# Kernel optimization log

Measured on AMD Instinct MI355X. Metric: run time of the kernel, lower is better.

Reference implementation:

```python
import jax, jax.numpy as jnp
import numpy as np

B, N, C_IN, C_OUT, E_DIM = 16, 1024, 64, 64, 4


def setup_inputs() -> dict:
    key = jax.random.key(0)
    ks = jax.random.split(key, 7)
    x = jax.random.normal(ks[0], (B, N, C_IN), dtype=jnp.float32)
    adj = jax.random.uniform(ks[1], (B, N, N), dtype=jnp.float32)
    edge_attr = jax.random.randint(ks[2], (B, N, N, 1), 0, E_DIM, dtype=jnp.int32)
    scale = 1.0 / np.sqrt(C_IN)
    W_rel = jax.random.normal(ks[3], (C_IN, C_OUT), dtype=jnp.float32) * scale
    b_rel = jax.random.normal(ks[4], (C_OUT,), dtype=jnp.float32) * scale
    W_root = jax.random.normal(ks[5], (C_IN, C_OUT), dtype=jnp.float32) * scale
    w_edge = jax.random.normal(ks[6], (E_DIM,), dtype=jnp.float32)
    return {"x": x, "adj": adj, "edge_attr": edge_attr,
            "W_rel": W_rel, "b_rel": b_rel, "W_root": W_root, "w_edge": w_edge}


def reference(x, adj, edge_attr, W_rel, b_rel, W_root, w_edge):
    # one_hot(edge_attr) @ w_edge == gather of w_edge by edge type (same math,
    # avoids materializing the B x N x N x E_DIM one-hot tensor).
    e = w_edge[edge_attr[..., 0]]            # [B, N, N]
    adj_w = adj * e                           # weighted adjacency
    out = jnp.matmul(adj_w, x)                # [B, N, C_IN] aggregation (aggr='add')
    out = jnp.matmul(out, W_rel) + b_rel      # lin_rel
    out = out + jnp.matmul(x, W_root)         # lin_root (no bias)
    return out
```

## Files before the change

kernel.cpp:

```cpp
#include <hip/hip_runtime.h>

#define BB 16
#define NN 1024
#define CC 64
#define TJ 128
#define IR 32
#define AW_STRIDE 132

typedef __attribute__((address_space(3))) void lds_void_t;
typedef const __attribute__((address_space(1))) void gbl_void_t;

__device__ __forceinline__ void load_lds16(const void* g, void* l) {
    __builtin_amdgcn_global_load_lds((gbl_void_t*)g, (lds_void_t*)l, 16, 0, 0);
}

extern "C" __global__ __launch_bounds__(256)
void precompute_xw(const float* __restrict__ x, const float* __restrict__ W_rel,
                   const float* __restrict__ W_root,
                   float* __restrict__ xw, float* __restrict__ xr)
{
    __shared__ float wrel_s[64 * 64];
    __shared__ float wroot_s[64 * 64];
    __shared__ float x_s[16 * 68];

    const int t = threadIdx.x;
    #pragma unroll
    for (int k = 0; k < 4; ++k) {
        int i4 = t + 256 * k;
        ((float4*)wrel_s)[i4]  = ((const float4*)W_rel)[i4];
        ((float4*)wroot_s)[i4] = ((const float4*)W_root)[i4];
    }
    const int row0 = blockIdx.x * 16;
    {
        int r = t >> 4, c4 = t & 15;
        *(float4*)(x_s + r * 68 + c4 * 4) = ((const float4*)(x + (size_t)(row0 + r) * CC))[c4];
    }
    __syncthreads();

    const int c4 = t & 15;
    const int r  = t >> 4;
    float aw0 = 0.f, aw1 = 0.f, aw2 = 0.f, aw3 = 0.f;
    float ar0 = 0.f, ar1 = 0.f, ar2 = 0.f, ar3 = 0.f;
    const float* xrow = x_s + r * 68;
    #pragma unroll 8
    for (int k = 0; k < 64; ++k) {
        float xv = xrow[k];
        float4 wv = ((const float4*)(wrel_s  + k * 64))[c4];
        float4 rv = ((const float4*)(wroot_s + k * 64))[c4];
        aw0 += xv * wv.x; aw1 += xv * wv.y; aw2 += xv * wv.z; aw3 += xv * wv.w;
        ar0 += xv * rv.x; ar1 += xv * rv.y; ar2 += xv * rv.z; ar3 += xv * rv.w;
    }
    const size_t o4 = (size_t)(row0 + r) * (CC / 4) + c4;
    ((float4*)xw)[o4] = make_float4(aw0, aw1, aw2, aw3);
    ((float4*)xr)[o4] = make_float4(ar0, ar1, ar2, ar3);
}

extern "C" __global__ __launch_bounds__(256)
void gnn_agg(const float* __restrict__ adj, const int* __restrict__ ea,
             const float* __restrict__ w_edge, const float* __restrict__ b_rel,
             const float* __restrict__ xw, const float* __restrict__ xr,
             float* __restrict__ out)
{
    __shared__ float x_s[TJ * CC];
    __shared__ float aw_s[IR * AW_STRIDE];

    const int t   = threadIdx.x;
    const int bid = blockIdx.x;
    const int b   = bid >> 5;
    const int i0  = (bid & 31) * IR;

    const float w0 = w_edge[0], w1 = w_edge[1], w2 = w_edge[2], w3 = w_edge[3];
    const int c4 = t & 15;
    const int rr = t >> 4;

    float4 acc0 = make_float4(0.f, 0.f, 0.f, 0.f);
    float4 acc1 = make_float4(0.f, 0.f, 0.f, 0.f);

    const float* adj_base = adj + ((size_t)b * NN + i0) * NN;
    const int*   ea_base  = ea  + ((size_t)b * NN + i0) * NN;
    const float* xw_base  = xw + (size_t)b * NN * CC;

    for (int j0 = 0; j0 < NN; j0 += TJ) {
        {
            const char* src = (const char*)(xw_base + (size_t)j0 * CC);
            char* dst = (char*)x_s;
            #pragma unroll
            for (int k = 0; k < 8; ++k) {
                int off = (t + 256 * k) * 16;
                load_lds16(src + off, dst + off);
            }
        }
        #pragma unroll
        for (int k = 0; k < 4; ++k) {
            int i4  = t + 256 * k;
            int row = i4 >> 5;
            int j4  = i4 & 31;
            const float4 av = *(const float4*)(adj_base + (size_t)row * NN + j0 + j4 * 4);
            const int4   iv = *(const int4*)  (ea_base  + (size_t)row * NN + j0 + j4 * 4);
            float4 ev;
            ev.x = av.x * (iv.x == 0 ? w0 : iv.x == 1 ? w1 : iv.x == 2 ? w2 : w3);
            ev.y = av.y * (iv.y == 0 ? w0 : iv.y == 1 ? w1 : iv.y == 2 ? w2 : w3);
            ev.z = av.z * (iv.z == 0 ? w0 : iv.z == 1 ? w1 : iv.z == 2 ? w2 : w3);
            ev.w = av.w * (iv.w == 0 ? w0 : iv.w == 1 ? w1 : iv.w == 2 ? w2 : w3);
            *(float4*)(aw_s + row * AW_STRIDE + j4 * 4) = ev;
        }
        __syncthreads();

        const float* awr0 = aw_s + (2 * rr + 0) * AW_STRIDE;
        const float* awr1 = aw_s + (2 * rr + 1) * AW_STRIDE;
        #pragma unroll 8
        for (int j = 0; j < TJ; j += 4) {
            float4 a0 = *(const float4*)(awr0 + j);
            float4 a1 = *(const float4*)(awr1 + j);
            float4 xv0 = ((const float4*)(x_s + (j + 0) * CC))[c4];
            float4 xv1 = ((const float4*)(x_s + (j + 1) * CC))[c4];
            float4 xv2 = ((const float4*)(x_s + (j + 2) * CC))[c4];
            float4 xv3 = ((const float4*)(x_s + (j + 3) * CC))[c4];
            acc0.x += a0.x * xv0.x; acc0.y += a0.x * xv0.y; acc0.z += a0.x * xv0.z; acc0.w += a0.x * xv0.w;
            acc0.x += a0.y * xv1.x; acc0.y += a0.y * xv1.y; acc0.z += a0.y * xv1.z; acc0.w += a0.y * xv1.w;
            acc0.x += a0.z * xv2.x; acc0.y += a0.z * xv2.y; acc0.z += a0.z * xv2.z; acc0.w += a0.z * xv2.w;
            acc0.x += a0.w * xv3.x; acc0.y += a0.w * xv3.y; acc0.z += a0.w * xv3.z; acc0.w += a0.w * xv3.w;
            acc1.x += a1.x * xv0.x; acc1.y += a1.x * xv0.y; acc1.z += a1.x * xv0.z; acc1.w += a1.x * xv0.w;
            acc1.x += a1.y * xv1.x; acc1.y += a1.y * xv1.y; acc1.z += a1.y * xv1.z; acc1.w += a1.y * xv1.w;
            acc1.x += a1.z * xv2.x; acc1.y += a1.z * xv2.y; acc1.z += a1.z * xv2.z; acc1.w += a1.z * xv2.w;
            acc1.x += a1.w * xv3.x; acc1.y += a1.w * xv3.y; acc1.z += a1.w * xv3.z; acc1.w += a1.w * xv3.w;
        }
        __syncthreads();
    }

    const float4 bv = ((const float4*)b_rel)[c4];
    const size_t row_g = (size_t)b * NN + i0 + 2 * rr;
    const float4* xr4  = (const float4*)(xr  + row_g * CC) + c4;
    float4*       out4 = (float4*)      (out + row_g * CC) + c4;
    float4 r0 = xr4[0];
    float4 r1 = xr4[CC / 4];
    float4 o0 = make_float4(acc0.x + bv.x + r0.x, acc0.y + bv.y + r0.y,
                            acc0.z + bv.z + r0.z, acc0.w + bv.w + r0.w);
    float4 o1 = make_float4(acc1.x + bv.x + r1.x, acc1.y + bv.y + r1.y,
                            acc1.z + bv.z + r1.z, acc1.w + bv.w + r1.w);
    out4[0]      = o0;
    out4[CC / 4] = o1;
}

extern "C" void kernel_launch(void* const* d_in, const int* in_sizes, int n_in,
                              void* d_out, int out_size, void* d_ws, size_t ws_size,
                              hipStream_t stream) {
    const float* x      = (const float*)d_in[0];
    const float* adj    = (const float*)d_in[1];
    const int*   ea     = (const int*)  d_in[2];
    const float* W_rel  = (const float*)d_in[3];
    const float* b_rel  = (const float*)d_in[4];
    const float* W_root = (const float*)d_in[5];
    const float* w_edge = (const float*)d_in[6];
    float* out = (float*)d_out;

    float* xw = (float*)d_ws;
    float* xr = xw + (size_t)BB * NN * CC;

    precompute_xw<<<BB * NN / 16, 256, 0, stream>>>(x, W_rel, W_root, xw, xr);
    gnn_agg<<<BB * (NN / IR), 256, 0, stream>>>(adj, ea, w_edge, b_rel, xw, xr, out);
}
```

Baseline: 199.4 us.

## Aggregate with bf16 MFMA using pre-swizzled xW and split-K across waves

The aggregation kernel now uses 16x16x32 bf16 MFMA instructions instead of scalar fp32 FMAs. The precompute kernel writes xW_rel as bf16 in a fragment-swizzled layout and writes x·W_root plus bias directly into the output, so the second kernel accumulates into it. Each block handles 16 rows, with four waves splitting K and reducing through LDS. Edge weights come from a cubic polynomial instead of a select chain. This targets FP32 ALU throughput and LDS staging so the kernel is bound by streaming adj and edge_attr, at the cost of bf16 truncation error (plain truncation for adj products) and one extra read-modify-write of the output.

```diff
diff --git a/kernel.cpp b/kernel.cpp
--- a/kernel.cpp
+++ b/kernel.cpp
@@ -3,21 +3,20 @@
 #define BB 16
 #define NN 1024
 #define CC 64
-#define TJ 128
-#define IR 32
-#define AW_STRIDE 132
 
-typedef __attribute__((address_space(3))) void lds_void_t;
-typedef const __attribute__((address_space(1))) void gbl_void_t;
+typedef __attribute__((ext_vector_type(8))) short short8;
+typedef __attribute__((ext_vector_type(4))) float f32x4;
 
-__device__ __forceinline__ void load_lds16(const void* g, void* l) {
-    __builtin_amdgcn_global_load_lds((gbl_void_t*)g, (lds_void_t*)l, 16, 0, 0);
+__device__ __forceinline__ unsigned short bf16_rne(float f) {
+    unsigned u = __float_as_uint(f);
+    u += 0x7fffu + ((u >> 16) & 1u);
+    return (unsigned short)(u >> 16);
 }
 
 extern "C" __global__ __launch_bounds__(256)
-void precompute_xw(const float* __restrict__ x, const float* __restrict__ W_rel,
-                   const float* __restrict__ W_root,
-                   float* __restrict__ xw, float* __restrict__ xr)
+void precompute(const float* __restrict__ x, const float* __restrict__ W_rel,
+                const float* __restrict__ W_root, const float* __restrict__ b_rel,
+                unsigned short* __restrict__ xw_sw, float* __restrict__ out)
 {
     __shared__ float wrel_s[64 * 64];
     __shared__ float wroot_s[64 * 64];
@@ -50,96 +49,127 @@
         aw0 += xv * wv.x; aw1 += xv * wv.y; aw2 += xv * wv.z; aw3 += xv * wv.w;
         ar0 += xv * rv.x; ar1 += xv * rv.y; ar2 += xv * rv.z; ar3 += xv * rv.w;
     }
-    const size_t o4 = (size_t)(row0 + r) * (CC / 4) + c4;
-    ((float4*)xw)[o4] = make_float4(aw0, aw1, aw2, aw3);
-    ((float4*)xr)[o4] = make_float4(ar0, ar1, ar2, ar3);
+
+    const int row_g = row0 + r;
+    {
+        const float4 bv = ((const float4*)b_rel)[c4];
+        ((float4*)out)[(size_t)row_g * 16 + c4] =
+            make_float4(ar0 + bv.x, ar1 + bv.y, ar2 + bv.z, ar3 + bv.w);
+    }
+    {
+        const int b = row_g >> 10;
+        const int k = row_g & 1023;
+        const int kb = k >> 5;
+        const int qk = (k >> 3) & 3;
+        const int j  = k & 7;
+        const int c  = 4 * c4;
+        const int n0 = c >> 4;
+        const int n  = c & 15;
+        size_t off = ((size_t)b << 16) + (size_t)((kb * 4 + n0) << 9)
+                   + (size_t)((n + (qk << 4)) << 3) + j;
+        xw_sw[off]      = bf16_rne(aw0);
+        xw_sw[off + 8]  = bf16_rne(aw1);
+        xw_sw[off + 16] = bf16_rne(aw2);
+        xw_sw[off + 24] = bf16_rne(aw3);
+    }
 }
 
-extern "C" __global__ __launch_bounds__(256)
-void gnn_agg(const float* __restrict__ adj, const int* __restrict__ ea,
-             const float* __restrict__ w_edge, const float* __restrict__ b_rel,
-             const float* __restrict__ xw, const float* __restrict__ xr,
-             float* __restrict__ out)
+extern "C" __global__ __launch_bounds__(256, 4)
+void gnn_mfma(const float* __restrict__ adj, const int* __restrict__ ea,
+              const float* __restrict__ w_edge,
+              const unsigned short* __restrict__ xw_sw,
+              float* __restrict__ out)
 {
-    __shared__ float x_s[TJ * CC];
-    __shared__ float aw_s[IR * AW_STRIDE];
+    __shared__ float red_s[3 * 16 * 64];
 
-    const int t   = threadIdx.x;
-    const int bid = blockIdx.x;
-    const int b   = bid >> 5;
-    const int i0  = (bid & 31) * IR;
+    const int t    = threadIdx.x;
+    const int w    = t >> 6;
+    const int lane = t & 63;
+    const int m    = lane & 15;
+    const int q    = lane >> 4;
+    const int b     = blockIdx.x >> 6;
+    const int mtile = blockIdx.x & 63;
 
     const float w0 = w_edge[0], w1 = w_edge[1], w2 = w_edge[2], w3 = w_edge[3];
-    const int c4 = t & 15;
-    const int rr = t >> 4;
+    const float d1 = w1 - w0;
+    const float d2 = w2 - 2.f * w1 + w0;
+    const float d3 = w3 - 3.f * w2 + 3.f * w1 - w0;
+    const float c3 = d3 * (1.f / 6.f);
+    const float c2 = 0.5f * d2 - 0.5f * d3;
+    const float c1 = d1 - 0.5f * d2 + (1.f / 3.f) * d3;
+    const float c0 = w0;
 
-    float4 acc0 = make_float4(0.f, 0.f, 0.f, 0.f);
-    float4 acc1 = make_float4(0.f, 0.f, 0.f, 0.f);
+    const int row = (mtile << 4) + m;
+    const float* arow = adj + (((size_t)b << 10) + row) * NN + (w << 8) + (q << 3);
+    const int*   erow = ea  + (((size_t)b << 10) + row) * NN + (w << 8) + (q << 3);
+    const short8* xf  = (const short8*)(xw_sw + ((size_t)b << 16) + (w << 14)) + lane;
 
-    const float* adj_base = adj + ((size_t)b * NN + i0) * NN;
-    const int*   ea_base  = ea  + ((size_t)b * NN + i0) * NN;
-    const float* xw_base  = xw + (size_t)b * NN * CC;
+    f32x4 acc0 = {0.f, 0.f, 0.f, 0.f};
+    f32x4 acc1 = acc0, acc2 = acc0, acc3 = acc0;
 
-    for (int j0 = 0; j0 < NN; j0 += TJ) {
-        {
-            const char* src = (const char*)(xw_base + (size_t)j0 * CC);
-            char* dst = (char*)x_s;
+    #pragma unroll 2
+    for (int kk = 0; kk < 8; ++kk) {
+        const float* ap = arow + (kk << 5);
+        const int*   ep = erow + (kk << 5);
+        float4 a0 = *(const float4*)ap;
+        float4 a1 = *(const float4*)(ap + 4);
+        int4   e0 = *(const int4*)ep;
+        int4   e1 = *(const int4*)(ep + 4);
+
+        #define WSEL(e) __builtin_fmaf(__builtin_fmaf(__builtin_fmaf(c3, (float)(e), c2), (float)(e), c1), (float)(e), c0)
+        float p0 = a0.x * WSEL(e0.x);
+        float p1 = a0.y * WSEL(e0.y);
+        float p2 = a0.z * WSEL(e0.z);
+        float p3 = a0.w * WSEL(e0.w);
+        float p4 = a1.x * WSEL(e1.x);
+        float p5 = a1.y * WSEL(e1.y);
+        float p6 = a1.z * WSEL(e1.z);
+        float p7 = a1.w * WSEL(e1.w);
+        #undef WSEL
+
+        union { int i[4]; short8 s; } af;
+        af.i[0] = __builtin_amdgcn_perm(__float_as_uint(p1), __float_as_uint(p0), 0x07060302u);
+        af.i[1] = __builtin_amdgcn_perm(__float_as_uint(p3), __float_as_uint(p2), 0x07060302u);
+        af.i[2] = __builtin_amdgcn_perm(__float_as_uint(p5), __float_as_uint(p4), 0x07060302u);
+        af.i[3] = __builtin_amdgcn_perm(__float_as_uint(p7), __float_as_uint(p6), 0x07060302u);
+
+        short8 bf0 = xf[(kk * 4 + 0) * 64];
+        short8 bf1 = xf[(kk * 4 + 1) * 64];
+        short8 bf2 = xf[(kk * 4 + 2) * 64];
+        short8 bf3 = xf[(kk * 4 + 3) * 64];
+
+        acc0 = __builtin_amdgcn_mfma_f32_16x16x32_bf16(af.s, bf0, acc0, 0, 0, 0);
+        acc1 = __builtin_amdgcn_mfma_f32_16x16x32_bf16(af.s, bf1, acc1, 0, 0, 0);
+        acc2 = __builtin_amdgcn_mfma_f32_16x16x32_bf16(af.s, bf2, acc2, 0, 0, 0);
+        acc3 = __builtin_amdgcn_mfma_f32_16x16x32_bf16(af.s, bf3, acc3, 0, 0, 0);
+    }
+
+    if (w != 0) {
+        float* buf = red_s + (w - 1) * 1024;
+        #pragma unroll
+        for (int rg = 0; rg < 4; ++rg) {
+            int rbase = (q * 4 + rg) * 64 + m;
+            buf[rbase]      = acc0[rg];
+            buf[rbase + 16] = acc1[rg];
+            buf[rbase + 32] = acc2[rg];
+            buf[rbase + 48] = acc3[rg];
+        }
+    }
+    __syncthreads();
+    if (w == 0) {
+        float* obase = out + (((size_t)b << 10) + (mtile << 4)) * 64;
+        #pragma unroll
+        for (int rg = 0; rg < 4; ++rg) {
+            int rbase = (q * 4 + rg) * 64 + m;
             #pragma unroll
-            for (int k = 0; k < 8; ++k) {
-                int off = (t + 256 * k) * 16;
-                load_lds16(src + off, dst + off);
+            for (int n0 = 0; n0 < 4; ++n0) {
+                int idx = rbase + n0 * 16;
+                float v = (n0 == 0 ? acc0[rg] : n0 == 1 ? acc1[rg] : n0 == 2 ? acc2[rg] : acc3[rg]);
+                v += red_s[idx] + red_s[1024 + idx] + red_s[2048 + idx];
+                obase[idx] += v;
             }
         }
-        #pragma unroll
-        for (int k = 0; k < 4; ++k) {
-            int i4  = t + 256 * k;
-            int row = i4 >> 5;
-            int j4  = i4 & 31;
-            const float4 av = *(const float4*)(adj_base + (size_t)row * NN + j0 + j4 * 4);
-            const int4   iv = *(const int4*)  (ea_base  + (size_t)row * NN + j0 + j4 * 4);
-            float4 ev;
-            ev.x = av.x * (iv.x == 0 ? w0 : iv.x == 1 ? w1 : iv.x == 2 ? w2 : w3);
-            ev.y = av.y * (iv.y == 0 ? w0 : iv.y == 1 ? w1 : iv.y == 2 ? w2 : w3);
-            ev.z = av.z * (iv.z == 0 ? w0 : iv.z == 1 ? w1 : iv.z == 2 ? w2 : w3);
-            ev.w = av.w * (iv.w == 0 ? w0 : iv.w == 1 ? w1 : iv.w == 2 ? w2 : w3);
-            *(float4*)(aw_s + row * AW_STRIDE + j4 * 4) = ev;
-        }
-        __syncthreads();
-
-        const float* awr0 = aw_s + (2 * rr + 0) * AW_STRIDE;
-        const float* awr1 = aw_s + (2 * rr + 1) * AW_STRIDE;
-        #pragma unroll 8
-        for (int j = 0; j < TJ; j += 4) {
-            float4 a0 = *(const float4*)(awr0 + j);
-            float4 a1 = *(const float4*)(awr1 + j);
-            float4 xv0 = ((const float4*)(x_s + (j + 0) * CC))[c4];
-            float4 xv1 = ((const float4*)(x_s + (j + 1) * CC))[c4];
-            float4 xv2 = ((const float4*)(x_s + (j + 2) * CC))[c4];
-            float4 xv3 = ((const float4*)(x_s + (j + 3) * CC))[c4];
-            acc0.x += a0.x * xv0.x; acc0.y += a0.x * xv0.y; acc0.z += a0.x * xv0.z; acc0.w += a0.x * xv0.w;
-            acc0.x += a0.y * xv1.x; acc0.y += a0.y * xv1.y; acc0.z += a0.y * xv1.z; acc0.w += a0.y * xv1.w;
-            acc0.x += a0.z * xv2.x; acc0.y += a0.z * xv2.y; acc0.z += a0.z * xv2.z; acc0.w += a0.z * xv2.w;
-            acc0.x += a0.w * xv3.x; acc0.y += a0.w * xv3.y; acc0.z += a0.w * xv3.z; acc0.w += a0.w * xv3.w;
-            acc1.x += a1.x * xv0.x; acc1.y += a1.x * xv0.y; acc1.z += a1.x * xv0.z; acc1.w += a1.x * xv0.w;
-            acc1.x += a1.y * xv1.x; acc1.y += a1.y * xv1.y; acc1.z += a1.y * xv1.z; acc1.w += a1.y * xv1.w;
-            acc1.x += a1.z * xv2.x; acc1.y += a1.z * xv2.y; acc1.z += a1.z * xv2.z; acc1.w += a1.z * xv2.w;
-            acc1.x += a1.w * xv3.x; acc1.y += a1.w * xv3.y; acc1.z += a1.w * xv3.z; acc1.w += a1.w * xv3.w;
-        }
-        __syncthreads();
     }
-
-    const float4 bv = ((const float4*)b_rel)[c4];
-    const size_t row_g = (size_t)b * NN + i0 + 2 * rr;
-    const float4* xr4  = (const float4*)(xr  + row_g * CC) + c4;
-    float4*       out4 = (float4*)      (out + row_g * CC) + c4;
-    float4 r0 = xr4[0];
-    float4 r1 = xr4[CC / 4];
-    float4 o0 = make_float4(acc0.x + bv.x + r0.x, acc0.y + bv.y + r0.y,
-                            acc0.z + bv.z + r0.z, acc0.w + bv.w + r0.w);
-    float4 o1 = make_float4(acc1.x + bv.x + r1.x, acc1.y + bv.y + r1.y,
-                            acc1.z + bv.z + r1.z, acc1.w + bv.w + r1.w);
-    out4[0]      = o0;
-    out4[CC / 4] = o1;
 }
 
 extern "C" void kernel_launch(void* const* d_in, const int* in_sizes, int n_in,
@@ -154,9 +184,8 @@
     const float* w_edge = (const float*)d_in[6];
     float* out = (float*)d_out;
 
-    float* xw = (float*)d_ws;
-    float* xr = xw + (size_t)BB * NN * CC;
+    unsigned short* xw_sw = (unsigned short*)d_ws;
 
-    precompute_xw<<<BB * NN / 16, 256, 0, stream>>>(x, W_rel, W_root, xw, xr);
-    gnn_agg<<<BB * (NN / IR), 256, 0, stream>>>(adj, ea, w_edge, b_rel, xw, xr, out);
+    precompute<<<BB * NN / 16, 256, 0, stream>>>(x, W_rel, W_root, b_rel, xw_sw, out);
+    gnn_mfma<<<BB * (NN / 16), 256, 0, stream>>>(adj, ea, w_edge, xw_sw, out);
 }
```

Result: faster. 178.2 us (-10.6%).
